# Kernel optimization log

Measured on AMD Instinct MI355X. Metric: run time of the kernel, lower is better.

Reference implementation:

```python
import jax, jax.numpy as jnp
import numpy as np
import math

D_MODEL = 1024
NUM_HEADS = 16
DK = D_MODEL // NUM_HEADS
THETA = 10000.0


def _rope(x, cos, sin):
    # x: (..., S, dk); cos/sin: (S, dk//2). Interleaved (even/odd) rotation,
    # matching x1=x[...,0::2], x2=x[...,1::2] then re-interleave via stack.
    x1 = x[..., 0::2]
    x2 = x[..., 1::2]
    r1 = x1 * cos - x2 * sin
    r2 = x1 * sin + x2 * cos
    return jnp.stack((r1, r2), axis=-1).reshape(x.shape)


def setup_inputs() -> dict:
    key = jax.random.key(0)
    k1, k2, k3 = jax.random.split(key, 3)
    B, S = 2, 2048
    x = jax.random.normal(k1, (B, S, D_MODEL), dtype=jnp.float32)
    std_qkv = (2.0 / (D_MODEL + 3 * D_MODEL)) ** 0.5
    Wqkv = jax.random.normal(k2, (3 * D_MODEL, D_MODEL), dtype=jnp.float32) * std_qkv
    std_o = (2.0 / (D_MODEL + D_MODEL)) ** 0.5
    Wo = jax.random.normal(k3, (D_MODEL, D_MODEL), dtype=jnp.float32) * std_o
    return {"x": x, "Wqkv": Wqkv, "Wo": Wo}


def reference(x, Wqkv, Wo):
    B, S, D = x.shape
    # fused QKV projection: Linear stores W as (out, in), y = x @ W^T
    qkv = jnp.einsum('bsd,od->bso', x, Wqkv)  # (B, S, 3*D)
    # split order in the source rearrange is (three, numheads, dk)
    qkv = qkv.reshape(B, S, 3, NUM_HEADS, DK).transpose(2, 0, 3, 1, 4)  # (3,B,H,S,dk)
    q, k, v = qkv[0], qkv[1], qkv[2]

    # RoPE tables (registered buffers in the source, deterministic constants)
    inv_freqs = 1.0 / (THETA ** (jnp.arange(0, DK, 2, dtype=jnp.float32) / DK))
    t = jnp.arange(S, dtype=jnp.float32)
    freqs = t[:, None] * inv_freqs[None, :]  # (S, dk//2)
    cos, sin = jnp.cos(freqs), jnp.sin(freqs)
    q = _rope(q, cos, sin)
    k = _rope(k, cos, sin)

    # naive full-materialization causal attention
    scores = jnp.einsum('bhqd,bhkd->bhqk', q, k) / math.sqrt(DK)  # (B,H,S,S)
    causal = jnp.tril(jnp.ones((S, S), dtype=bool))
    scores = jnp.where(causal, scores, -jnp.inf)
    attn = jax.nn.softmax(scores, axis=-1)
    out = jnp.einsum('bhqk,bhkd->bhqd', attn, v)  # (B,H,S,dk)
    out = out.transpose(0, 2, 1, 3).reshape(B, S, D)  # concat heads
    return jnp.einsum('bsd,od->bso', out, Wo)
```

## Files before the change

### kernel.cpp

```cpp
#include <hip/hip_runtime.h>
#include <hip/hip_bf16.h>
#include <cstdint>
#include <cstddef>


typedef unsigned short u16;
typedef unsigned int   u32;

typedef float f32x4 __attribute__((ext_vector_type(4)));
typedef short frag_t __attribute__((ext_vector_type(8)));

__device__ __forceinline__ f32x4 mfma16(frag_t a, frag_t b, f32x4 c) {
  return __builtin_amdgcn_mfma_f32_16x16x32_bf16(a, b, c, 0, 0, 0);
}

typedef __attribute__((address_space(1))) void as1_void;
typedef __attribute__((address_space(3))) void as3_void;
__device__ __forceinline__ void gload_lds16(const void* g, void* l) {
  __builtin_amdgcn_global_load_lds((as1_void*)g, (as3_void*)l, 16, 0, 0);
}

__device__ __forceinline__ u16 f2bf(float f) {
  u32 u = __builtin_bit_cast(u32, f);
  u += 0x7fffu + ((u >> 16) & 1u);
  return (u16)(u >> 16);
}
__device__ __forceinline__ float bf2f(u16 h) {
  u32 u = ((u32)h) << 16;
  return __builtin_bit_cast(float, u);
}
__device__ __forceinline__ u16 bf16u(float f) {
  __hip_bfloat16 h = __float2bfloat16(f);
  u16 u;
  __builtin_memcpy(&u, &h, 2);
  return u;
}
__device__ __forceinline__ float exp2_hw(float x) {
  float r;
  asm("v_exp_f32 %0, %1" : "=v"(r) : "v"(x));
  return r;
}

static constexpr int Bb = 2, Ss = 2048, Hh = 16, Dd = 1024;
static constexpr int Mm = Bb * Ss;
static constexpr int NT = Ss / 64;

__global__ __launch_bounds__(256) void cvt_f32_bf16(const float* __restrict__ in,
                                                    u16* __restrict__ out, int n4) {
  for (int i = blockIdx.x * blockDim.x + threadIdx.x; i < n4;
       i += gridDim.x * blockDim.x) {
    float4 v = ((const float4*)in)[i];
    ushort4 o;
    o.x = f2bf(v.x); o.y = f2bf(v.y); o.z = f2bf(v.z); o.w = f2bf(v.w);
    ((ushort4*)out)[i] = o;
  }
}

__global__ __launch_bounds__(256) void build_rope_table(float2* __restrict__ tab) {
  int i = blockIdx.x * blockDim.x + threadIdx.x;
  if (i >= Ss * 32) return;
  int s = i >> 5, j = i & 31;
  const float log2_theta_over_32 = 0.41524101186091903f;
  float inv = exp2f(-(float)j * log2_theta_over_32);
  float fr = (float)s * inv;
  float sn, cs;
  sincosf(fr, &sn, &cs);
  tab[i] = make_float2(cs, sn);
}

template <bool OUT_BF16>
__global__ __launch_bounds__(256) void gemm_bt_kernel(const u16* __restrict__ A,
                                                      const u16* __restrict__ Bm,
                                                      void* __restrict__ Cv,
                                                      int Mdim, int Ndim, int Kdim) {
  __shared__ __align__(16) u16 As[2][128 * 64];
  __shared__ __align__(16) u16 Bs[2][128 * 64];
  const int tid = threadIdx.x;
  const int lane = tid & 63, wid = tid >> 6;
  const int wr = wid >> 1, wc = wid & 1;
  const int lr = lane & 15, lg = lane >> 4;

  const int nwg = gridDim.x * gridDim.y;
  const int orig = blockIdx.y * gridDim.x + blockIdx.x;
  const int cpx = nwg >> 3;
  const int swz = (orig & 7) * cpx + (orig >> 3);
  const int bx = swz % gridDim.x, by = swz / gridDim.x;
  const int m0 = by * 128, n0 = bx * 128;

  f32x4 acc[4][4] = {};

  const int rowA = lane >> 3;
  const int colu = (lane & 7) * 8;

  auto stage = [&](int buf, int kt) {
#pragma unroll
    for (int i = 0; i < 4; i++) {
      int chunk = wid * 4 + i;
      const u16* ga = A + (size_t)(m0 + chunk * 8 + rowA) * Kdim + kt + colu;
      gload_lds16(ga, &As[buf][chunk * 512]);
      const u16* gb = Bm + (size_t)(n0 + chunk * 8 + rowA) * Kdim + kt + colu;
      gload_lds16(gb, &Bs[buf][chunk * 512]);
    }
  };

  stage(0, 0);
  __syncthreads();

  int cur = 0;
  for (int kt = 0; kt < Kdim; kt += 64) {
    if (kt + 64 < Kdim) stage(cur ^ 1, kt + 64);

#pragma unroll
    for (int ks = 0; ks < 2; ks++) {
      frag_t a[4], b[4];
#pragma unroll
      for (int mt = 0; mt < 4; mt++)
        a[mt] = *(const frag_t*)&As[cur][(wr * 64 + mt * 16 + lr) * 64 + ks * 32 + lg * 8];
#pragma unroll
      for (int nt = 0; nt < 4; nt++)
        b[nt] = *(const frag_t*)&Bs[cur][(wc * 64 + nt * 16 + lr) * 64 + ks * 32 + lg * 8];
#pragma unroll
      for (int mt = 0; mt < 4; mt++)
#pragma unroll
        for (int nt = 0; nt < 4; nt++)
          acc[mt][nt] = mfma16(a[mt], b[nt], acc[mt][nt]);
    }

    __syncthreads();
    cur ^= 1;
  }

#pragma unroll
  for (int mt = 0; mt < 4; mt++)
#pragma unroll
    for (int nt = 0; nt < 4; nt++)
#pragma unroll
      for (int r = 0; r < 4; r++) {
        size_t row = (size_t)(m0 + wr * 64 + mt * 16 + lg * 4 + r);
        size_t col = (size_t)(n0 + wc * 64 + nt * 16 + lr);
        if (OUT_BF16)
          ((u16*)Cv)[row * Ndim + col] = f2bf(acc[mt][nt][r]);
        else
          ((float*)Cv)[row * Ndim + col] = acc[mt][nt][r];
      }
}

__global__ __launch_bounds__(256) void rope_kernel(const u16* __restrict__ qkv,
                                                   const float2* __restrict__ tab,
                                                   u16* __restrict__ q_r,
                                                   u16* __restrict__ k_r,
                                                   u16* __restrict__ vt) {
  const int bh = blockIdx.y, b = bh >> 4, h = bh & 15;
  const int s0 = blockIdx.x * 64;
  const int t = threadIdx.x;
  __shared__ __align__(16) u16 Vls[64 * 72];

  const int srow = t >> 2, c4 = t & 3;
  const int s = s0 + srow;
  const size_t rowbase = (size_t)(b * Ss + s) * 3072 + h * 64 + c4 * 16;

  u16 xq[16] __attribute__((aligned(16)));
  u16 xk[16] __attribute__((aligned(16)));
  u16 xv[16] __attribute__((aligned(16)));
  *(uint4*)&xq[0] = *(const uint4*)(qkv + rowbase);
  *(uint4*)&xq[8] = *(const uint4*)(qkv + rowbase + 8);
  *(uint4*)&xk[0] = *(const uint4*)(qkv + rowbase + 1024);
  *(uint4*)&xk[8] = *(const uint4*)(qkv + rowbase + 1024 + 8);
  *(uint4*)&xv[0] = *(const uint4*)(qkv + rowbase + 2048);
  *(uint4*)&xv[8] = *(const uint4*)(qkv + rowbase + 2048 + 8);

  u16 oq[16] __attribute__((aligned(16)));
  u16 ok[16] __attribute__((aligned(16)));
  const int j0 = c4 * 8;
  const float qscale = 0.125f * 1.4426950408889634f;
#pragma unroll
  for (int p = 0; p < 8; p++) {
    float2 cs = tab[s * 32 + j0 + p];
    float q1 = bf2f(xq[2 * p]), q2 = bf2f(xq[2 * p + 1]);
    float k1 = bf2f(xk[2 * p]), k2 = bf2f(xk[2 * p + 1]);
    oq[2 * p]     = f2bf((q1 * cs.x - q2 * cs.y) * qscale);
    oq[2 * p + 1] = f2bf((q1 * cs.y + q2 * cs.x) * qscale);
    ok[2 * p]     = f2bf(k1 * cs.x - k2 * cs.y);
    ok[2 * p + 1] = f2bf(k1 * cs.y + k2 * cs.x);
  }
  const size_t obase = ((size_t)bh * Ss + s) * 64 + c4 * 16;
  *(uint4*)(q_r + obase)     = *(uint4*)&oq[0];
  *(uint4*)(q_r + obase + 8) = *(uint4*)&oq[8];
  *(uint4*)(k_r + obase)     = *(uint4*)&ok[0];
  *(uint4*)(k_r + obase + 8) = *(uint4*)&ok[8];

  *(uint4*)&Vls[srow * 72 + c4 * 16]     = *(uint4*)&xv[0];
  *(uint4*)&Vls[srow * 72 + c4 * 16 + 8] = *(uint4*)&xv[8];
  __syncthreads();
  const int d = t >> 2, cq = t & 3;
  u16 ov[16] __attribute__((aligned(16)));
#pragma unroll
  for (int i = 0; i < 16; i++) ov[i] = Vls[(cq * 16 + i) * 72 + d];
  const size_t vbase = ((size_t)bh * 64 + d) * Ss + s0 + cq * 16;
  *(uint4*)(vt + vbase)     = *(uint4*)&ov[0];
  *(uint4*)(vt + vbase + 8) = *(uint4*)&ov[8];
}

__global__ __launch_bounds__(512, 4) void attn_kernel(const u16* __restrict__ q_r,
                                                      const u16* __restrict__ k_r,
                                                      const u16* __restrict__ vt,
                                                      u16* __restrict__ o) {
  const int pr = blockIdx.x;
  const int bh = blockIdx.y;
  const int b = bh >> 4, h = bh & 15;
  const int tid = threadIdx.x;
  const int lane = tid & 63, w = tid >> 6;
  const int ww = w & 3;
  const int lr = lane & 15, lg = lane >> 4;

  const int qt = (w < 4) ? pr : (NT - 1 - pr);
  const int qtB = NT - 1 - pr;

  __shared__ __align__(16) u16 Ks[2][64 * 72];
  __shared__ __align__(16) u16 Vs[2][64 * 72];
  __shared__ __align__(16) u16 Ps[8][16 * 72];

  const size_t kvbase = (size_t)bh * Ss * 64;
  const size_t vtbase = (size_t)bh * 64 * Ss;
  u16* Pw = &Ps[w][0];
  const int qrow = ww * 16 + lr;

  frag_t q0f, q1f;
  {
    const u16* qa = q_r + kvbase + (size_t)(qt * 64 + qrow) * 64 + lg * 8;
    q0f = *(const frag_t*)qa;
    q1f = *(const frag_t*)(qa + 32);
  }

  const int srow = tid >> 3, scol = (tid & 7) * 8;
  uint4 kreg, vreg;
  const u16* kp = k_r + kvbase;
  const u16* vp = vt + vtbase;

  auto issue = [&](int kt) {
    kreg = *(const uint4*)(kp + (size_t)(kt * 64 + srow) * 64 + scol);
    vreg = *(const uint4*)(vp + (size_t)srow * Ss + kt * 64 + scol);
  };
  auto commit = [&](int buf) {
    *(uint4*)&Ks[buf][srow * 72 + scol] = kreg;
    *(uint4*)&Vs[buf][srow * 72 + scol] = vreg;
  };

  f32x4 oacc[4] = {};
  float l_run = 0.f;

  issue(0);
  commit(0);
  __syncthreads();

  for (int kt = 0; kt <= qtB; kt++) {
    const int cur = kt & 1;
    const bool last = (kt == qtB);
    if (!last) issue(kt + 1);

    if (kt <= qt) {
      f32x4 sa[4];
      __builtin_amdgcn_s_setprio(1);
#pragma unroll
      for (int kf = 0; kf < 4; kf++) {
        frag_t k0 = *(const frag_t*)&Ks[cur][(kf * 16 + lr) * 72 + lg * 8];
        frag_t k1 = *(const frag_t*)&Ks[cur][(kf * 16 + lr) * 72 + 32 + lg * 8];
        sa[kf] = mfma16(k0, q0f, f32x4{0.f, 0.f, 0.f, 0.f});
        sa[kf] = mfma16(k1, q1f, sa[kf]);
      }
      __builtin_amdgcn_s_setprio(0);

      if (kt == qt) {
#pragma unroll
        for (int kf = 0; kf < 4; kf++)
#pragma unroll
          for (int r = 0; r < 4; r++)
            if (kf * 16 + lg * 4 + r > qrow) sa[kf][r] = -1e30f;
      }

      float ls = 0.f;
#pragma unroll
      for (int kf = 0; kf < 4; kf++) {
        float p0 = exp2_hw(sa[kf][0]), p1 = exp2_hw(sa[kf][1]);
        float p2 = exp2_hw(sa[kf][2]), p3 = exp2_hw(sa[kf][3]);
        ls += (p0 + p1) + (p2 + p3);
        ushort4 w4;
        w4.x = bf16u(p0); w4.y = bf16u(p1); w4.z = bf16u(p2); w4.w = bf16u(p3);
        *(ushort4*)&Pw[lr * 72 + kf * 16 + lg * 4] = w4;
      }
      l_run += ls;

      __builtin_amdgcn_s_setprio(1);
#pragma unroll
      for (int ks = 0; ks < 2; ks++) {
        frag_t pa = *(const frag_t*)&Pw[lr * 72 + ks * 32 + lg * 8];
#pragma unroll
        for (int df = 0; df < 4; df++) {
          frag_t bv = *(const frag_t*)&Vs[cur][(df * 16 + lr) * 72 + ks * 32 + lg * 8];
          oacc[df] = mfma16(pa, bv, oacc[df]);
        }
      }
      __builtin_amdgcn_s_setprio(0);
    }

    if (!last) commit(cur ^ 1);
    __syncthreads();
  }

  l_run += __shfl_xor(l_run, 16);
  l_run += __shfl_xor(l_run, 32);
#pragma unroll
  for (int r = 0; r < 4; r++) {
    float il = 1.0f / __shfl(l_run, lg * 4 + r);
    size_t row = (size_t)b * Ss + qt * 64 + ww * 16 + lg * 4 + r;
#pragma unroll
    for (int df = 0; df < 4; df++)
      o[row * 1024 + h * 64 + df * 16 + lr] = f2bf(oacc[df][r] * il);
  }
}

extern "C" void kernel_launch(void* const* d_in, const int* in_sizes, int n_in,
                              void* d_out, int out_size, void* d_ws, size_t ws_size,
                              hipStream_t stream) {
  const float* x    = (const float*)d_in[0];
  const float* Wqkv = (const float*)d_in[1];
  const float* Wo   = (const float*)d_in[2];
  float* out = (float*)d_out;
  char* ws = (char*)d_ws;

  constexpr size_t TAB_OFF  = 0;
  constexpr size_t XB_OFF   = TAB_OFF + 524288;
  constexpr size_t WQB_OFF  = XB_OFF + 8388608;
  constexpr size_t WOB_OFF  = WQB_OFF + 6291456;
  constexpr size_t QKV_OFF  = WOB_OFF + 2097152;
  constexpr size_t QR_OFF   = QKV_OFF + 25165824;
  constexpr size_t KR_OFF   = QR_OFF + 8388608;
  constexpr size_t VT_OFF   = KR_OFF + 8388608;
  constexpr size_t AO_OFF   = VT_OFF + 8388608;

  float2* tab = (float2*)(ws + TAB_OFF);
  u16* xb     = (u16*)(ws + XB_OFF);
  u16* wqkvb  = (u16*)(ws + WQB_OFF);
  u16* wob    = (u16*)(ws + WOB_OFF);
  u16* qkv    = (u16*)(ws + QKV_OFF);
  u16* q_r    = (u16*)(ws + QR_OFF);
  u16* k_r    = (u16*)(ws + KR_OFF);
  u16* vt     = (u16*)(ws + VT_OFF);
  u16* ao     = (u16*)(ws + AO_OFF);

  build_rope_table<<<256, 256, 0, stream>>>(tab);
  cvt_f32_bf16<<<2048, 256, 0, stream>>>(x, xb, Mm * Dd / 4);
  cvt_f32_bf16<<<1536, 256, 0, stream>>>(Wqkv, wqkvb, 3 * Dd * Dd / 4);
  cvt_f32_bf16<<<512, 256, 0, stream>>>(Wo, wob, Dd * Dd / 4);

  gemm_bt_kernel<true><<<dim3(3 * Dd / 128, Mm / 128), 256, 0, stream>>>(
      xb, wqkvb, qkv, Mm, 3 * Dd, Dd);

  rope_kernel<<<dim3(Ss / 64, Bb * Hh), 256, 0, stream>>>(qkv, tab, q_r, k_r, vt);

  attn_kernel<<<dim3(NT / 2, Bb * Hh), 512, 0, stream>>>(q_r, k_r, vt, ao);

  gemm_bt_kernel<false><<<dim3(Dd / 128, Mm / 128), 256, 0, stream>>>(
      ao, wob, out, Mm, Dd, Dd);
}
```

Baseline: 145.6 us.

## Swizzle GEMM LDS layout and prefetch two K-tiles ahead with vmcnt waits

```diff
diff --git a/kernel.cpp b/kernel.cpp
--- a/kernel.cpp
+++ b/kernel.cpp
@@ -90,7 +90,7 @@
   f32x4 acc[4][4] = {};
 
   const int rowA = lane >> 3;
-  const int colu = (lane & 7) * 8;
+  const int colu = ((lane & 7) ^ rowA) * 8;
 
   auto stage = [&](int buf, int kt) {
 #pragma unroll
@@ -103,22 +103,29 @@
     }
   };
 
+  const int niter = Kdim >> 6;
+
   stage(0, 0);
-  __syncthreads();
-
+  stage(1, 64);
+  asm volatile("s_waitcnt vmcnt(8)" ::: "memory");
+  __builtin_amdgcn_sched_barrier(0);
+  __builtin_amdgcn_s_barrier();
+  __builtin_amdgcn_sched_barrier(0);
+
+  const int rsw = (lr & 7) * 8;
   int cur = 0;
-  for (int kt = 0; kt < Kdim; kt += 64) {
-    if (kt + 64 < Kdim) stage(cur ^ 1, kt + 64);
-
+  for (int it = 0; it < niter; ++it) {
 #pragma unroll
     for (int ks = 0; ks < 2; ks++) {
       frag_t a[4], b[4];
 #pragma unroll
       for (int mt = 0; mt < 4; mt++)
-        a[mt] = *(const frag_t*)&As[cur][(wr * 64 + mt * 16 + lr) * 64 + ks * 32 + lg * 8];
+        a[mt] = *(const frag_t*)&As[cur][(wr * 64 + mt * 16 + lr) * 64 +
+                                         ((ks * 32 + lg * 8) ^ rsw)];
 #pragma unroll
       for (int nt = 0; nt < 4; nt++)
-        b[nt] = *(const frag_t*)&Bs[cur][(wc * 64 + nt * 16 + lr) * 64 + ks * 32 + lg * 8];
+        b[nt] = *(const frag_t*)&Bs[cur][(wc * 64 + nt * 16 + lr) * 64 +
+                                         ((ks * 32 + lg * 8) ^ rsw)];
 #pragma unroll
       for (int mt = 0; mt < 4; mt++)
 #pragma unroll
@@ -126,8 +133,20 @@
           acc[mt][nt] = mfma16(a[mt], b[nt], acc[mt][nt]);
     }
 
-    __syncthreads();
-    cur ^= 1;
+    if (it + 1 < niter) {
+      __builtin_amdgcn_s_barrier();
+      __builtin_amdgcn_sched_barrier(0);
+      if (it + 2 < niter) {
+        stage(cur, (it + 2) << 6);
+        asm volatile("s_waitcnt vmcnt(8)" ::: "memory");
+      } else {
+        asm volatile("s_waitcnt vmcnt(0)" ::: "memory");
+      }
+      __builtin_amdgcn_sched_barrier(0);
+      __builtin_amdgcn_s_barrier();
+      __builtin_amdgcn_sched_barrier(0);
+      cur ^= 1;
+    }
   }
 
 #pragma unroll
```

Measured after the change: 131.7 us. 9.6% less time.
